# Performance work log

Hardware: AMD Instinct MI355X
Metric: run time of the kernel (lower is better)

Reference implementation:

```python
import jax, jax.numpy as jnp
import numpy as np

EPS = 1e-5  # torch BatchNorm2d default eps


def _conv_bn(x, w, b, gamma, beta, mean, var):
    # 1x1 conv -> relu -> BatchNorm (eval mode, running stats), per Conv2d helper
    y = jnp.einsum('bchw,oc->bohw', x, w) + b[None, :, None, None]
    y = jax.nn.relu(y)
    inv = gamma / jnp.sqrt(var + EPS)
    return y * inv[None, :, None, None] + (beta - mean * inv)[None, :, None, None]


def setup_inputs() -> dict:
    key = jax.random.key(0)
    ks = jax.random.split(key, 32)
    B, C, H, W = 4, 128, 64, 64
    d = {'x': jax.random.normal(ks[0], (B, C, H, W), jnp.float32)}
    i = 1
    for p in ('theta', 'phi', 'g', 'out'):
        d[f'{p}_w'] = jax.random.normal(ks[i], (C, C), jnp.float32) * 0.05; i += 1
        d[f'{p}_b'] = jax.random.normal(ks[i], (C,), jnp.float32) * 0.05; i += 1
        d[f'{p}_gamma'] = jax.random.uniform(ks[i], (C,), jnp.float32, 0.5, 1.5); i += 1
        d[f'{p}_beta'] = jax.random.normal(ks[i], (C,), jnp.float32) * 0.05; i += 1
        d[f'{p}_mean'] = jax.random.normal(ks[i], (C,), jnp.float32) * 0.05; i += 1
        d[f'{p}_var'] = jax.random.uniform(ks[i], (C,), jnp.float32, 0.5, 1.5); i += 1
    return d


def reference(x, theta_w, theta_b, theta_gamma, theta_beta, theta_mean, theta_var,
              phi_w, phi_b, phi_gamma, phi_beta, phi_mean, phi_var,
              g_w, g_b, g_gamma, g_beta, g_mean, g_var,
              out_w, out_b, out_gamma, out_beta, out_mean, out_var):
    B, C, H, W = x.shape
    N = H * W
    # faithful to torch: .view(B, -1, C) is a raw reshape of the (B,C,H,W) buffer
    theta = _conv_bn(x, theta_w, theta_b, theta_gamma, theta_beta, theta_mean, theta_var).reshape(B, N, C)
    phi = _conv_bn(x, phi_w, phi_b, phi_gamma, phi_beta, phi_mean, phi_var).reshape(B, N, C)
    g = _conv_bn(x, g_w, g_b, g_gamma, g_beta, g_mean, g_var).reshape(B, N, C)
    attn = jax.nn.softmax(jnp.einsum('bnc,bmc->bnm', theta, phi), axis=2)  # (B,N,N)
    # Dropout1d is identity in eval mode
    t = jnp.einsum('bnm,bmc->bnc', attn, g).reshape(B, C, H, W)
    t = jnp.einsum('bchw,oc->bohw', t, out_w) + out_b[None, :, None, None]
    inv = out_gamma / jnp.sqrt(out_var + EPS)
    t = t * inv[None, :, None, None] + (out_beta - out_mean * inv)[None, :, None, None]
    t = jax.nn.relu(t)
    return x + t, attn
```

## Files before the change

kernel.cpp:

```cpp
#include <hip/hip_runtime.h>


typedef _Float16 f16;
typedef __attribute__((ext_vector_type(8))) _Float16 f16x8;
typedef __attribute__((ext_vector_type(4))) float f32x4;

#define CC 128
#define NN 4096
#define BB 4
#define NC (NN * CC)
#define EPS_BN 1e-5f

#define OFF_THETA  (0ull)
#define OFF_PHI    (4ull << 20)
#define OFF_G      (8ull << 20)
#define OFF_GT     (12ull << 20)
#define OFF_PSTAT  (16ull << 20)
#define OFF_STAT   (OFF_PSTAT + (1ull << 19))
#define OFF_TPART  (17ull << 20)
#define OFF_T      (33ull << 20)

__global__ __launch_bounds__(256) void k_prep(
    const float* __restrict__ x,
    const float* __restrict__ t_w, const float* __restrict__ t_b,
    const float* __restrict__ t_ga, const float* __restrict__ t_be,
    const float* __restrict__ t_me, const float* __restrict__ t_va,
    const float* __restrict__ p_w, const float* __restrict__ p_b,
    const float* __restrict__ p_ga, const float* __restrict__ p_be,
    const float* __restrict__ p_me, const float* __restrict__ p_va,
    const float* __restrict__ g_w, const float* __restrict__ g_b,
    const float* __restrict__ g_ga, const float* __restrict__ g_be,
    const float* __restrict__ g_me, const float* __restrict__ g_va,
    f16* __restrict__ th, f16* __restrict__ ph, f16* __restrict__ gh)
{
  const int s0 = blockIdx.x * 512 + threadIdx.x;
  const int s1 = s0 + 256;
  const int o0 = blockIdx.y * 8;
  const int b  = blockIdx.z;
  const float* xb = x + (size_t)b * NC;

  float acc[3][8][2];
#pragma unroll
  for (int br = 0; br < 3; ++br)
#pragma unroll
    for (int j = 0; j < 8; ++j) { acc[br][j][0] = 0.f; acc[br][j][1] = 0.f; }

#pragma unroll 4
  for (int c = 0; c < CC; ++c) {
    float x0 = xb[c * NN + s0];
    float x1 = xb[c * NN + s1];
#pragma unroll
    for (int j = 0; j < 8; ++j) {
      float w0 = t_w[(o0 + j) * CC + c];
      float w1 = p_w[(o0 + j) * CC + c];
      float w2 = g_w[(o0 + j) * CC + c];
      acc[0][j][0] += w0 * x0; acc[0][j][1] += w0 * x1;
      acc[1][j][0] += w1 * x0; acc[1][j][1] += w1 * x1;
      acc[2][j][0] += w2 * x0; acc[2][j][1] += w2 * x1;
    }
  }

  f16* outs[3] = { th, ph, gh };
  const float* bi[3] = { t_b,  p_b,  g_b  };
  const float* ga[3] = { t_ga, p_ga, g_ga };
  const float* be[3] = { t_be, p_be, g_be };
  const float* me[3] = { t_me, p_me, g_me };
  const float* va[3] = { t_va, p_va, g_va };
#pragma unroll
  for (int br = 0; br < 3; ++br) {
#pragma unroll
    for (int j = 0; j < 8; ++j) {
      int o = o0 + j;
      float inv = ga[br][o] * rsqrtf(va[br][o] + EPS_BN);
      float add = be[br][o] - me[br][o] * inv;
      float bs  = bi[br][o];
      float y0 = fmaxf(acc[br][j][0] + bs, 0.f) * inv + add;
      float y1 = fmaxf(acc[br][j][1] + bs, 0.f) * inv + add;
      f16* op = outs[br] + (size_t)b * NC + (size_t)o * NN;
      op[s0] = (f16)y0;
      op[s1] = (f16)y1;
    }
  }
}

__global__ __launch_bounds__(256) void k_tr_g(const f16* __restrict__ gh,
                                              f16* __restrict__ gt)
{
  __shared__ f16 tile[64][72];
  const int b   = blockIdx.z;
  const int m0  = blockIdx.x * 64;
  const int c20 = blockIdx.y * 64;
  const f16* gb_ = gh + (size_t)b * NC;
  f16* gtb = gt + (size_t)b * NC;
  const int t = threadIdx.x;
  {
    const int mr = t >> 2, co = (t & 3) * 16;
    f16x8 v0 = *(const f16x8*)(gb_ + (size_t)(m0 + mr) * CC + c20 + co);
    f16x8 v1 = *(const f16x8*)(gb_ + (size_t)(m0 + mr) * CC + c20 + co + 8);
#pragma unroll
    for (int j = 0; j < 8; ++j) tile[co + j][mr] = v0[j];
#pragma unroll
    for (int j = 0; j < 8; ++j) tile[co + 8 + j][mr] = v1[j];
  }
  __syncthreads();
  {
    const int cr = t >> 2, mo = (t & 3) * 16;
    f16x8 w0 = *(const f16x8*)(&tile[cr][mo]);
    f16x8 w1 = *(const f16x8*)(&tile[cr][mo + 8]);
    *(f16x8*)(gtb + (size_t)(c20 + cr) * NN + m0 + mo)     = w0;
    *(f16x8*)(gtb + (size_t)(c20 + cr) * NN + m0 + mo + 8) = w1;
  }
}

__global__ __launch_bounds__(64, 4) void k_sweep1(
    const f16* __restrict__ th, const f16* __restrict__ ph_,
    float2* __restrict__ pstat)
{
  const int bid = blockIdx.x;
  const int b = bid & 3, chunk = (bid >> 2) & 3, rb = bid >> 4;
  const int lane = threadIdx.x & 63;
  const int lr = lane & 15, lg = lane >> 4;
  const int n0 = rb * 32;
  const f16* tb_ = th  + (size_t)b * NC;
  const f16* pb_ = ph_ + (size_t)b * NC;

  f16x8 a[2][4];
#pragma unroll
  for (int tr = 0; tr < 2; ++tr)
#pragma unroll
    for (int kk = 0; kk < 4; ++kk)
      a[tr][kk] = *(const f16x8*)(tb_ + (size_t)(n0 + tr * 16 + lr) * CC + kk * 32 + lg * 8);

  float mreg[2][4], lreg[2][4];
#pragma unroll
  for (int tr = 0; tr < 2; ++tr)
#pragma unroll
    for (int r = 0; r < 4; ++r) { mreg[tr][r] = -1e30f; lreg[tr][r] = 0.f; }

  const int mbase = chunk * 1024;
  for (int t = 0; t < 64; ++t) {
    const int mc = mbase + t * 16;
    f16x8 bf[4];
#pragma unroll
    for (int kk = 0; kk < 4; ++kk)
      bf[kk] = *(const f16x8*)(pb_ + (size_t)(mc + lr) * CC + kk * 32 + lg * 8);
#pragma unroll
    for (int tr = 0; tr < 2; ++tr) {
      f32x4 d = {0.f, 0.f, 0.f, 0.f};
#pragma unroll
      for (int kk = 0; kk < 4; ++kk)
        d = __builtin_amdgcn_mfma_f32_16x16x32_f16(a[tr][kk], bf[kk], d, 0, 0, 0);
#pragma unroll
      for (int r = 0; r < 4; ++r) {
        float z  = d[r];
        float mn = fmaxf(mreg[tr][r], z);
        lreg[tr][r] = lreg[tr][r] * __expf(mreg[tr][r] - mn) + __expf(z - mn);
        mreg[tr][r] = mn;
      }
    }
  }
#pragma unroll
  for (int off = 1; off < 16; off <<= 1) {
#pragma unroll
    for (int tr = 0; tr < 2; ++tr)
#pragma unroll
      for (int r = 0; r < 4; ++r) {
        float mo = __shfl_xor(mreg[tr][r], off);
        float lo = __shfl_xor(lreg[tr][r], off);
        float mn = fmaxf(mreg[tr][r], mo);
        lreg[tr][r] = lreg[tr][r] * __expf(mreg[tr][r] - mn) + lo * __expf(mo - mn);
        mreg[tr][r] = mn;
      }
  }
  if (lr == 0) {
#pragma unroll
    for (int tr = 0; tr < 2; ++tr)
#pragma unroll
      for (int r = 0; r < 4; ++r) {
        int n = n0 + tr * 16 + lg * 4 + r;
        pstat[(size_t)(chunk * BB + b) * NN + n] = make_float2(mreg[tr][r], lreg[tr][r]);
      }
  }
}

__global__ void k_merge_stats(const float2* __restrict__ pstat,
                              float2* __restrict__ stat)
{
  int i = blockIdx.x * 256 + threadIdx.x;
  float2 s0 = pstat[i];
  float2 s1 = pstat[(size_t)BB * NN + i];
  float2 s2 = pstat[(size_t)2 * BB * NN + i];
  float2 s3 = pstat[(size_t)3 * BB * NN + i];
  float m = fmaxf(fmaxf(s0.x, s1.x), fmaxf(s2.x, s3.x));
  float L = s0.y * __expf(s0.x - m) + s1.y * __expf(s1.x - m) +
            s2.y * __expf(s2.x - m) + s3.y * __expf(s3.x - m);
  stat[i] = make_float2(m, 1.0f / L);
}

__global__ __launch_bounds__(64, 2) void k_sweep2(
    const f16* __restrict__ th, const f16* __restrict__ ph_,
    const f16* __restrict__ gt, const float2* __restrict__ stat,
    float* __restrict__ attn, f16* __restrict__ tpart)
{
  __shared__ f16 plds[32 * 40];
  const int bid = blockIdx.x;
  const int b = bid & 3, chunk = (bid >> 2) & 3, rb = bid >> 4;
  const int lane = threadIdx.x & 63;
  const int lr = lane & 15, lg = lane >> 4;
  const int n0 = rb * 32;
  const f16* tb_ = th  + (size_t)b * NC;
  const f16* pb_ = ph_ + (size_t)b * NC;
  const f16* gb_ = gt  + (size_t)b * NC;

  f16x8 a[2][4];
#pragma unroll
  for (int tr = 0; tr < 2; ++tr)
#pragma unroll
    for (int kk = 0; kk < 4; ++kk)
      a[tr][kk] = *(const f16x8*)(tb_ + (size_t)(n0 + tr * 16 + lr) * CC + kk * 32 + lg * 8);

  float M[2][4], Li[2][4];
#pragma unroll
  for (int tr = 0; tr < 2; ++tr)
#pragma unroll
    for (int r = 0; r < 4; ++r) {
      float2 st = stat[(size_t)b * NN + n0 + tr * 16 + lg * 4 + r];
      M[tr][r] = st.x; Li[tr][r] = st.y;
    }

  f32x4 tacc[2][8];
#pragma unroll
  for (int tr = 0; tr < 2; ++tr)
#pragma unroll
    for (int ct = 0; ct < 8; ++ct) tacc[tr][ct] = (f32x4){0.f, 0.f, 0.f, 0.f};

  float* attn_b = attn + (size_t)b * NN * NN;
  const int mbase = chunk * 1024;

  for (int grp = 0; grp < 32; ++grp) {
    const int m0 = mbase + grp * 32;
#pragma unroll
    for (int sub = 0; sub < 2; ++sub) {
      const int mc = m0 + sub * 16;
      f16x8 bf[4];
#pragma unroll
      for (int kk = 0; kk < 4; ++kk)
        bf[kk] = *(const f16x8*)(pb_ + (size_t)(mc + lr) * CC + kk * 32 + lg * 8);
#pragma unroll
      for (int tr = 0; tr < 2; ++tr) {
        f32x4 d = {0.f, 0.f, 0.f, 0.f};
#pragma unroll
        for (int kk = 0; kk < 4; ++kk)
          d = __builtin_amdgcn_mfma_f32_16x16x32_f16(a[tr][kk], bf[kk], d, 0, 0, 0);
#pragma unroll
        for (int r = 0; r < 4; ++r) {
          float p = __expf(d[r] - M[tr][r]) * Li[tr][r];
          attn_b[(size_t)(n0 + tr * 16 + lg * 4 + r) * NN + mc + lr] = p;
          plds[(tr * 16 + lg * 4 + r) * 40 + sub * 16 + lr] = (f16)p;
        }
      }
    }
    f16x8 pa[2];
#pragma unroll
    for (int tr = 0; tr < 2; ++tr)
      pa[tr] = *(const f16x8*)(&plds[(tr * 16 + lr) * 40 + lg * 8]);
#pragma unroll
    for (int ct = 0; ct < 8; ++ct) {
      f16x8 gbf = *(const f16x8*)(gb_ + (size_t)(ct * 16 + lr) * NN + m0 + lg * 8);
#pragma unroll
      for (int tr = 0; tr < 2; ++tr)
        tacc[tr][ct] = __builtin_amdgcn_mfma_f32_16x16x32_f16(pa[tr], gbf, tacc[tr][ct], 0, 0, 0);
    }
  }

  f16* tp = tpart + (size_t)(chunk * BB + b) * NC;
#pragma unroll
  for (int tr = 0; tr < 2; ++tr)
#pragma unroll
    for (int ct = 0; ct < 8; ++ct)
#pragma unroll
      for (int r = 0; r < 4; ++r)
        tp[(size_t)(n0 + tr * 16 + lg * 4 + r) * CC + ct * 16 + lr] = (f16)tacc[tr][ct][r];
}

__global__ void k_merge_t(const f16* __restrict__ tpart, f16* __restrict__ t_h)
{
  int i = blockIdx.x * 256 + threadIdx.x;
  size_t base = (size_t)i * 8;
  f16x8 v0 = *(const f16x8*)(tpart + base);
  f16x8 v1 = *(const f16x8*)(tpart + (size_t)BB * NC + base);
  f16x8 v2 = *(const f16x8*)(tpart + (size_t)2 * BB * NC + base);
  f16x8 v3 = *(const f16x8*)(tpart + (size_t)3 * BB * NC + base);
  f16x8 o;
#pragma unroll
  for (int j = 0; j < 8; ++j)
    o[j] = (f16)((float)v0[j] + (float)v1[j] + (float)v2[j] + (float)v3[j]);
  *(f16x8*)(t_h + base) = o;
}

__global__ __launch_bounds__(256) void k_outconv(
    const float* __restrict__ x, const f16* __restrict__ t_h,
    const float* __restrict__ o_w, const float* __restrict__ o_b,
    const float* __restrict__ o_ga, const float* __restrict__ o_be,
    const float* __restrict__ o_me, const float* __restrict__ o_va,
    float* __restrict__ out0)
{
  const int s0 = blockIdx.x * 512 + threadIdx.x;
  const int s1 = s0 + 256;
  const int o0 = blockIdx.y * 8;
  const int b  = blockIdx.z;
  const f16* tb_ = t_h + (size_t)b * NC;
  float acc[8][2];
#pragma unroll
  for (int j = 0; j < 8; ++j) { acc[j][0] = 0.f; acc[j][1] = 0.f; }

#pragma unroll 4
  for (int c = 0; c < CC; ++c) {
    float t0 = (float)tb_[c * NN + s0];
    float t1 = (float)tb_[c * NN + s1];
#pragma unroll
    for (int j = 0; j < 8; ++j) {
      float w = o_w[(o0 + j) * CC + c];
      acc[j][0] += w * t0; acc[j][1] += w * t1;
    }
  }
#pragma unroll
  for (int j = 0; j < 8; ++j) {
    int o = o0 + j;
    float inv = o_ga[o] * rsqrtf(o_va[o] + EPS_BN);
    float add = o_be[o] - o_me[o] * inv;
    float y0 = fmaxf((acc[j][0] + o_b[o]) * inv + add, 0.f);
    float y1 = fmaxf((acc[j][1] + o_b[o]) * inv + add, 0.f);
    size_t base = (size_t)(b * CC + o) * NN;
    out0[base + s0] = x[base + s0] + y0;
    out0[base + s1] = x[base + s1] + y1;
  }
}

extern "C" void kernel_launch(void* const* d_in, const int* in_sizes, int n_in,
                              void* d_out, int out_size, void* d_ws, size_t ws_size,
                              hipStream_t stream)
{
  (void)in_sizes; (void)n_in; (void)out_size; (void)ws_size;
  const float* x    = (const float*)d_in[0];
  const float* t_w  = (const float*)d_in[1];
  const float* t_b  = (const float*)d_in[2];
  const float* t_ga = (const float*)d_in[3];
  const float* t_be = (const float*)d_in[4];
  const float* t_me = (const float*)d_in[5];
  const float* t_va = (const float*)d_in[6];
  const float* p_w  = (const float*)d_in[7];
  const float* p_b  = (const float*)d_in[8];
  const float* p_ga = (const float*)d_in[9];
  const float* p_be = (const float*)d_in[10];
  const float* p_me = (const float*)d_in[11];
  const float* p_va = (const float*)d_in[12];
  const float* g_w  = (const float*)d_in[13];
  const float* g_b  = (const float*)d_in[14];
  const float* g_ga = (const float*)d_in[15];
  const float* g_be = (const float*)d_in[16];
  const float* g_me = (const float*)d_in[17];
  const float* g_va = (const float*)d_in[18];
  const float* o_w  = (const float*)d_in[19];
  const float* o_b  = (const float*)d_in[20];
  const float* o_ga = (const float*)d_in[21];
  const float* o_be = (const float*)d_in[22];
  const float* o_me = (const float*)d_in[23];
  const float* o_va = (const float*)d_in[24];

  char* ws = (char*)d_ws;
  f16*    th    = (f16*)   (ws + OFF_THETA);
  f16*    ph    = (f16*)   (ws + OFF_PHI);
  f16*    gh    = (f16*)   (ws + OFF_G);
  f16*    gt    = (f16*)   (ws + OFF_GT);
  float2* pstat = (float2*)(ws + OFF_PSTAT);
  float2* stat  = (float2*)(ws + OFF_STAT);
  f16*    tpart = (f16*)   (ws + OFF_TPART);
  f16*    t_h   = (f16*)   (ws + OFF_T);

  float* out0 = (float*)d_out;
  float* attn = out0 + (size_t)BB * CC * NN;

  k_prep<<<dim3(8, 16, BB), 256, 0, stream>>>(
      x, t_w, t_b, t_ga, t_be, t_me, t_va,
         p_w, p_b, p_ga, p_be, p_me, p_va,
         g_w, g_b, g_ga, g_be, g_me, g_va, th, ph, gh);
  k_tr_g<<<dim3(64, 2, BB), 256, 0, stream>>>(gh, gt);
  k_sweep1<<<2048, 64, 0, stream>>>(th, ph, pstat);
  k_merge_stats<<<64, 256, 0, stream>>>(pstat, stat);
  k_sweep2<<<2048, 64, 0, stream>>>(th, ph, gt, stat, attn, tpart);
  k_merge_t<<<1024, 256, 0, stream>>>(tpart, t_h);
  k_outconv<<<dim3(8, 16, BB), 256, 0, stream>>>(
      x, t_h, o_w, o_b, o_ga, o_be, o_me, o_va, out0);
}
```

Baseline: 598.3 us.

## Restructure attention sweeps into 4-wave blocks with LDS-staged coalesced attn stores

Both sweep kernels move from one-wave blocks handling 32 rows to 256-thread blocks where each wave handles 16 rows, so a block covers 64 rows. Sweep2 stages fp32 probabilities in a double-buffered LDS tile and writes attn with coalesced 16-byte nontemporal stores. It stores a single log-sum-exp per row instead of max plus inverse sum. Sweep1 uses a lazy max update that rescales only when the new score exceeds the running max by more than 8, which cuts exp calls. The 1x1 conv kernels drop to one pixel per thread with twice the grid, and the workspace offsets are compacted so pstat overlaps the dead g buffer.

```diff
diff --git a/kernel.cpp b/kernel.cpp
--- a/kernel.cpp
+++ b/kernel.cpp
@@ -11,14 +11,14 @@
 #define NC (NN * CC)
 #define EPS_BN 1e-5f
 
-#define OFF_THETA  (0ull)
-#define OFF_PHI    (4ull << 20)
-#define OFF_G      (8ull << 20)
-#define OFF_GT     (12ull << 20)
-#define OFF_PSTAT  (16ull << 20)
-#define OFF_STAT   (OFF_PSTAT + (1ull << 19))
-#define OFF_TPART  (17ull << 20)
-#define OFF_T      (33ull << 20)
+#define OFF_THETA (0ull)
+#define OFF_PHI   (4ull << 20)
+#define OFF_G     (8ull << 20)
+#define OFF_GT    (12ull << 20)
+#define OFF_PSTAT (8ull << 20)
+#define OFF_STAT  (OFF_PSTAT + (1ull << 19))
+#define OFF_TPART (16ull << 20)
+#define OFF_T     (32ull << 20)
 
 __global__ __launch_bounds__(256) void k_prep(
     const float* __restrict__ x,
@@ -33,30 +33,25 @@
     const float* __restrict__ g_me, const float* __restrict__ g_va,
     f16* __restrict__ th, f16* __restrict__ ph, f16* __restrict__ gh)
 {
-  const int s0 = blockIdx.x * 512 + threadIdx.x;
-  const int s1 = s0 + 256;
+  const int s  = blockIdx.x * 256 + threadIdx.x;
   const int o0 = blockIdx.y * 8;
   const int b  = blockIdx.z;
   const float* xb = x + (size_t)b * NC;
 
-  float acc[3][8][2];
+  float acc[3][8];
 #pragma unroll
   for (int br = 0; br < 3; ++br)
 #pragma unroll
-    for (int j = 0; j < 8; ++j) { acc[br][j][0] = 0.f; acc[br][j][1] = 0.f; }
+    for (int j = 0; j < 8; ++j) acc[br][j] = 0.f;
 
 #pragma unroll 4
   for (int c = 0; c < CC; ++c) {
-    float x0 = xb[c * NN + s0];
-    float x1 = xb[c * NN + s1];
+    float xv = xb[c * NN + s];
 #pragma unroll
     for (int j = 0; j < 8; ++j) {
-      float w0 = t_w[(o0 + j) * CC + c];
-      float w1 = p_w[(o0 + j) * CC + c];
-      float w2 = g_w[(o0 + j) * CC + c];
-      acc[0][j][0] += w0 * x0; acc[0][j][1] += w0 * x1;
-      acc[1][j][0] += w1 * x0; acc[1][j][1] += w1 * x1;
-      acc[2][j][0] += w2 * x0; acc[2][j][1] += w2 * x1;
+      acc[0][j] += t_w[(o0 + j) * CC + c] * xv;
+      acc[1][j] += p_w[(o0 + j) * CC + c] * xv;
+      acc[2][j] += g_w[(o0 + j) * CC + c] * xv;
     }
   }
 
@@ -73,12 +68,8 @@
       int o = o0 + j;
       float inv = ga[br][o] * rsqrtf(va[br][o] + EPS_BN);
       float add = be[br][o] - me[br][o] * inv;
-      float bs  = bi[br][o];
-      float y0 = fmaxf(acc[br][j][0] + bs, 0.f) * inv + add;
-      float y1 = fmaxf(acc[br][j][1] + bs, 0.f) * inv + add;
-      f16* op = outs[br] + (size_t)b * NC + (size_t)o * NN;
-      op[s0] = (f16)y0;
-      op[s1] = (f16)y1;
+      float y = fmaxf(acc[br][j] + bi[br][o], 0.f) * inv + add;
+      outs[br][(size_t)b * NC + (size_t)o * NN + s] = (f16)y;
     }
   }
 }
@@ -112,30 +103,26 @@
   }
 }
 
-__global__ __launch_bounds__(64, 4) void k_sweep1(
+__global__ __launch_bounds__(256, 4) void k_sweep1(
     const f16* __restrict__ th, const f16* __restrict__ ph_,
     float2* __restrict__ pstat)
 {
   const int bid = blockIdx.x;
   const int b = bid & 3, chunk = (bid >> 2) & 3, rb = bid >> 4;
-  const int lane = threadIdx.x & 63;
-  const int lr = lane & 15, lg = lane >> 4;
-  const int n0 = rb * 32;
+  const int tid = threadIdx.x, w = tid >> 6;
+  const int lane = tid & 63, lr = lane & 15, lg = lane >> 4;
+  const int wn0 = rb * 64 + w * 16;
   const f16* tb_ = th  + (size_t)b * NC;
   const f16* pb_ = ph_ + (size_t)b * NC;
 
-  f16x8 a[2][4];
-#pragma unroll
-  for (int tr = 0; tr < 2; ++tr)
-#pragma unroll
-    for (int kk = 0; kk < 4; ++kk)
-      a[tr][kk] = *(const f16x8*)(tb_ + (size_t)(n0 + tr * 16 + lr) * CC + kk * 32 + lg * 8);
-
-  float mreg[2][4], lreg[2][4];
-#pragma unroll
-  for (int tr = 0; tr < 2; ++tr)
-#pragma unroll
-    for (int r = 0; r < 4; ++r) { mreg[tr][r] = -1e30f; lreg[tr][r] = 0.f; }
+  f16x8 a[4];
+#pragma unroll
+  for (int kk = 0; kk < 4; ++kk)
+    a[kk] = *(const f16x8*)(tb_ + (size_t)(wn0 + lr) * CC + kk * 32 + lg * 8);
+
+  float m[4], l[4];
+#pragma unroll
+  for (int r = 0; r < 4; ++r) { m[r] = -1e30f; l[r] = 0.f; }
 
   const int mbase = chunk * 1024;
   for (int t = 0; t < 64; ++t) {
@@ -144,47 +131,37 @@
 #pragma unroll
     for (int kk = 0; kk < 4; ++kk)
       bf[kk] = *(const f16x8*)(pb_ + (size_t)(mc + lr) * CC + kk * 32 + lg * 8);
-#pragma unroll
-    for (int tr = 0; tr < 2; ++tr) {
-      f32x4 d = {0.f, 0.f, 0.f, 0.f};
-#pragma unroll
-      for (int kk = 0; kk < 4; ++kk)
-        d = __builtin_amdgcn_mfma_f32_16x16x32_f16(a[tr][kk], bf[kk], d, 0, 0, 0);
-#pragma unroll
-      for (int r = 0; r < 4; ++r) {
-        float z  = d[r];
-        float mn = fmaxf(mreg[tr][r], z);
-        lreg[tr][r] = lreg[tr][r] * __expf(mreg[tr][r] - mn) + __expf(z - mn);
-        mreg[tr][r] = mn;
-      }
+    f32x4 d = {0.f, 0.f, 0.f, 0.f};
+#pragma unroll
+    for (int kk = 0; kk < 4; ++kk)
+      d = __builtin_amdgcn_mfma_f32_16x16x32_f16(a[kk], bf[kk], d, 0, 0, 0);
+#pragma unroll
+    for (int r = 0; r < 4; ++r) {
+      float dd = d[r] - m[r];
+      if (dd > 8.f) { l[r] = l[r] * __expf(-dd) + 1.f; m[r] = d[r]; }
+      else          { l[r] += __expf(dd); }
     }
   }
 #pragma unroll
   for (int off = 1; off < 16; off <<= 1) {
 #pragma unroll
-    for (int tr = 0; tr < 2; ++tr)
-#pragma unroll
-      for (int r = 0; r < 4; ++r) {
-        float mo = __shfl_xor(mreg[tr][r], off);
-        float lo = __shfl_xor(lreg[tr][r], off);
-        float mn = fmaxf(mreg[tr][r], mo);
-        lreg[tr][r] = lreg[tr][r] * __expf(mreg[tr][r] - mn) + lo * __expf(mo - mn);
-        mreg[tr][r] = mn;
-      }
+    for (int r = 0; r < 4; ++r) {
+      float mo = __shfl_xor(m[r], off);
+      float lo = __shfl_xor(l[r], off);
+      float mn = fmaxf(m[r], mo);
+      l[r] = l[r] * __expf(m[r] - mn) + lo * __expf(mo - mn);
+      m[r] = mn;
+    }
   }
   if (lr == 0) {
 #pragma unroll
-    for (int tr = 0; tr < 2; ++tr)
-#pragma unroll
-      for (int r = 0; r < 4; ++r) {
-        int n = n0 + tr * 16 + lg * 4 + r;
-        pstat[(size_t)(chunk * BB + b) * NN + n] = make_float2(mreg[tr][r], lreg[tr][r]);
-      }
+    for (int r = 0; r < 4; ++r)
+      pstat[(size_t)(chunk * BB + b) * NN + wn0 + lg * 4 + r] = make_float2(m[r], l[r]);
   }
 }
 
 __global__ void k_merge_stats(const float2* __restrict__ pstat,
-                              float2* __restrict__ stat)
+                              float* __restrict__ stat)
 {
   int i = blockIdx.x * 256 + threadIdx.x;
   float2 s0 = pstat[i];
@@ -194,51 +171,47 @@
   float m = fmaxf(fmaxf(s0.x, s1.x), fmaxf(s2.x, s3.x));
   float L = s0.y * __expf(s0.x - m) + s1.y * __expf(s1.x - m) +
             s2.y * __expf(s2.x - m) + s3.y * __expf(s3.x - m);
-  stat[i] = make_float2(m, 1.0f / L);
-}
-
-__global__ __launch_bounds__(64, 2) void k_sweep2(
+  stat[i] = m + __logf(L);
+}
+
+#define PSTRIDE 36
+#define PSZ (64 * PSTRIDE)
+
+__global__ __launch_bounds__(256, 4) void k_sweep2(
     const f16* __restrict__ th, const f16* __restrict__ ph_,
-    const f16* __restrict__ gt, const float2* __restrict__ stat,
+    const f16* __restrict__ gt, const float* __restrict__ stat,
     float* __restrict__ attn, f16* __restrict__ tpart)
 {
-  __shared__ f16 plds[32 * 40];
+  __shared__ float plds[2 * PSZ];
   const int bid = blockIdx.x;
   const int b = bid & 3, chunk = (bid >> 2) & 3, rb = bid >> 4;
-  const int lane = threadIdx.x & 63;
-  const int lr = lane & 15, lg = lane >> 4;
-  const int n0 = rb * 32;
+  const int tid = threadIdx.x, w = tid >> 6;
+  const int lane = tid & 63, lr = lane & 15, lg = lane >> 4;
+  const int n0 = rb * 64, wn0 = n0 + w * 16;
   const f16* tb_ = th  + (size_t)b * NC;
   const f16* pb_ = ph_ + (size_t)b * NC;
   const f16* gb_ = gt  + (size_t)b * NC;
 
-  f16x8 a[2][4];
-#pragma unroll
-  for (int tr = 0; tr < 2; ++tr)
-#pragma unroll
-    for (int kk = 0; kk < 4; ++kk)
-      a[tr][kk] = *(const f16x8*)(tb_ + (size_t)(n0 + tr * 16 + lr) * CC + kk * 32 + lg * 8);
-
-  float M[2][4], Li[2][4];
-#pragma unroll
-  for (int tr = 0; tr < 2; ++tr)
-#pragma unroll
-    for (int r = 0; r < 4; ++r) {
-      float2 st = stat[(size_t)b * NN + n0 + tr * 16 + lg * 4 + r];
-      M[tr][r] = st.x; Li[tr][r] = st.y;
-    }
-
-  f32x4 tacc[2][8];
-#pragma unroll
-  for (int tr = 0; tr < 2; ++tr)
-#pragma unroll
-    for (int ct = 0; ct < 8; ++ct) tacc[tr][ct] = (f32x4){0.f, 0.f, 0.f, 0.f};
+  f16x8 aq[4];
+#pragma unroll
+  for (int kk = 0; kk < 4; ++kk)
+    aq[kk] = *(const f16x8*)(tb_ + (size_t)(wn0 + lr) * CC + kk * 32 + lg * 8);
+
+  float S[4];
+#pragma unroll
+  for (int r = 0; r < 4; ++r) S[r] = stat[(size_t)b * NN + wn0 + lg * 4 + r];
+
+  f32x4 tacc[8];
+#pragma unroll
+  for (int ct = 0; ct < 8; ++ct) tacc[ct] = (f32x4){0.f, 0.f, 0.f, 0.f};
 
   float* attn_b = attn + (size_t)b * NN * NN;
   const int mbase = chunk * 1024;
+  const int arow = tid >> 2, acol = (tid & 3) * 8;
 
   for (int grp = 0; grp < 32; ++grp) {
     const int m0 = mbase + grp * 32;
+    float* pb = plds + (grp & 1) * PSZ;
 #pragma unroll
     for (int sub = 0; sub < 2; ++sub) {
       const int mc = m0 + sub * 16;
@@ -246,41 +219,38 @@
 #pragma unroll
       for (int kk = 0; kk < 4; ++kk)
         bf[kk] = *(const f16x8*)(pb_ + (size_t)(mc + lr) * CC + kk * 32 + lg * 8);
-#pragma unroll
-      for (int tr = 0; tr < 2; ++tr) {
-        f32x4 d = {0.f, 0.f, 0.f, 0.f};
-#pragma unroll
-        for (int kk = 0; kk < 4; ++kk)
-          d = __builtin_amdgcn_mfma_f32_16x16x32_f16(a[tr][kk], bf[kk], d, 0, 0, 0);
-#pragma unroll
-        for (int r = 0; r < 4; ++r) {
-          float p = __expf(d[r] - M[tr][r]) * Li[tr][r];
-          attn_b[(size_t)(n0 + tr * 16 + lg * 4 + r) * NN + mc + lr] = p;
-          plds[(tr * 16 + lg * 4 + r) * 40 + sub * 16 + lr] = (f16)p;
-        }
-      }
-    }
-    f16x8 pa[2];
-#pragma unroll
-    for (int tr = 0; tr < 2; ++tr)
-      pa[tr] = *(const f16x8*)(&plds[(tr * 16 + lr) * 40 + lg * 8]);
+      f32x4 d = {0.f, 0.f, 0.f, 0.f};
+#pragma unroll
+      for (int kk = 0; kk < 4; ++kk)
+        d = __builtin_amdgcn_mfma_f32_16x16x32_f16(aq[kk], bf[kk], d, 0, 0, 0);
+#pragma unroll
+      for (int r = 0; r < 4; ++r)
+        pb[(w * 16 + lg * 4 + r) * PSTRIDE + sub * 16 + lr] = __expf(d[r] - S[r]);
+    }
+    __syncthreads();
+    f32x4 o0 = *(const f32x4*)&pb[arow * PSTRIDE + acol];
+    f32x4 o1 = *(const f32x4*)&pb[arow * PSTRIDE + acol + 4];
+    f32x4 q0 = *(const f32x4*)&pb[(w * 16 + lr) * PSTRIDE + lg * 8];
+    f32x4 q1 = *(const f32x4*)&pb[(w * 16 + lr) * PSTRIDE + lg * 8 + 4];
+    f16x8 pa;
+#pragma unroll
+    for (int e = 0; e < 4; ++e) { pa[e] = (f16)q0[e]; pa[4 + e] = (f16)q1[e]; }
+    float* ab = attn_b + (size_t)(n0 + arow) * NN + m0 + acol;
+    __builtin_nontemporal_store(o0, (f32x4*)ab);
+    __builtin_nontemporal_store(o1, (f32x4*)(ab + 4));
 #pragma unroll
     for (int ct = 0; ct < 8; ++ct) {
       f16x8 gbf = *(const f16x8*)(gb_ + (size_t)(ct * 16 + lr) * NN + m0 + lg * 8);
-#pragma unroll
-      for (int tr = 0; tr < 2; ++tr)
-        tacc[tr][ct] = __builtin_amdgcn_mfma_f32_16x16x32_f16(pa[tr], gbf, tacc[tr][ct], 0, 0, 0);
+      tacc[ct] = __builtin_amdgcn_mfma_f32_16x16x32_f16(pa, gbf, tacc[ct], 0, 0, 0);
     }
   }
 
   f16* tp = tpart + (size_t)(chunk * BB + b) * NC;
 #pragma unroll
-  for (int tr = 0; tr < 2; ++tr)
-#pragma unroll
-    for (int ct = 0; ct < 8; ++ct)
-#pragma unroll
-      for (int r = 0; r < 4; ++r)
-        tp[(size_t)(n0 + tr * 16 + lg * 4 + r) * CC + ct * 16 + lr] = (f16)tacc[tr][ct][r];
+  for (int ct = 0; ct < 8; ++ct)
+#pragma unroll
+    for (int r = 0; r < 4; ++r)
+      tp[(size_t)(wn0 + lg * 4 + r) * CC + ct * 16 + lr] = (f16)tacc[ct][r];
 }
 
 __global__ void k_merge_t(const f16* __restrict__ tpart, f16* __restrict__ t_h)
@@ -305,35 +275,29 @@
     const float* __restrict__ o_me, const float* __restrict__ o_va,
     float* __restrict__ out0)
 {
-  const int s0 = blockIdx.x * 512 + threadIdx.x;
-  const int s1 = s0 + 256;
+  const int s  = blockIdx.x * 256 + threadIdx.x;
   const int o0 = blockIdx.y * 8;
   const int b  = blockIdx.z;
   const f16* tb_ = t_h + (size_t)b * NC;
-  float acc[8][2];
-#pragma unroll
-  for (int j = 0; j < 8; ++j) { acc[j][0] = 0.f; acc[j][1] = 0.f; }
+  float acc[8];
+#pragma unroll
+  for (int j = 0; j < 8; ++j) acc[j] = 0.f;
 
 #pragma unroll 4
   for (int c = 0; c < CC; ++c) {
-    float t0 = (float)tb_[c * NN + s0];
-    float t1 = (float)tb_[c * NN + s1];
-#pragma unroll
-    for (int j = 0; j < 8; ++j) {
-      float w = o_w[(o0 + j) * CC + c];
-      acc[j][0] += w * t0; acc[j][1] += w * t1;
-    }
+    float tv = (float)tb_[c * NN + s];
+#pragma unroll
+    for (int j = 0; j < 8; ++j)
+      acc[j] += o_w[(o0 + j) * CC + c] * tv;
   }
 #pragma unroll
   for (int j = 0; j < 8; ++j) {
     int o = o0 + j;
     float inv = o_ga[o] * rsqrtf(o_va[o] + EPS_BN);
     float add = o_be[o] - o_me[o] * inv;
-    float y0 = fmaxf((acc[j][0] + o_b[o]) * inv + add, 0.f);
-    float y1 = fmaxf((acc[j][1] + o_b[o]) * inv + add, 0.f);
-    size_t base = (size_t)(b * CC + o) * NN;
-    out0[base + s0] = x[base + s0] + y0;
-    out0[base + s1] = x[base + s1] + y1;
+    float y = fmaxf((acc[j] + o_b[o]) * inv + add, 0.f);
+    size_t idx = (size_t)(b * CC + o) * NN + s;
+    out0[idx] = x[idx] + y;
   }
 }
 
@@ -374,22 +338,22 @@
   f16*    gh    = (f16*)   (ws + OFF_G);
   f16*    gt    = (f16*)   (ws + OFF_GT);
   float2* pstat = (float2*)(ws + OFF_PSTAT);
-  float2* stat  = (float2*)(ws + OFF_STAT);
+  float*  stat  = (float*) (ws + OFF_STAT);
   f16*    tpart = (f16*)   (ws + OFF_TPART);
   f16*    t_h   = (f16*)   (ws + OFF_T);
 
   float* out0 = (float*)d_out;
   float* attn = out0 + (size_t)BB * CC * NN;
 
-  k_prep<<<dim3(8, 16, BB), 256, 0, stream>>>(
+  k_prep<<<dim3(16, 16, BB), 256, 0, stream>>>(
       x, t_w, t_b, t_ga, t_be, t_me, t_va,
          p_w, p_b, p_ga, p_be, p_me, p_va,
          g_w, g_b, g_ga, g_be, g_me, g_va, th, ph, gh);
   k_tr_g<<<dim3(64, 2, BB), 256, 0, stream>>>(gh, gt);
-  k_sweep1<<<2048, 64, 0, stream>>>(th, ph, pstat);
+  k_sweep1<<<1024, 256, 0, stream>>>(th, ph, pstat);
   k_merge_stats<<<64, 256, 0, stream>>>(pstat, stat);
-  k_sweep2<<<2048, 64, 0, stream>>>(th, ph, gt, stat, attn, tpart);
+  k_sweep2<<<1024, 256, 0, stream>>>(th, ph, gt, stat, attn, tpart);
   k_merge_t<<<1024, 256, 0, stream>>>(tpart, t_h);
-  k_outconv<<<dim3(8, 16, BB), 256, 0, stream>>>(
+  k_outconv<<<dim3(16, 16, BB), 256, 0, stream>>>(
       x, t_h, o_w, o_b, o_ga, o_be, o_me, o_va, out0);
 }
```

New measurement: 702.9 us. 17.5% more time.
